# Kernel tuning notes

Hardware: AMD Instinct MI355X
Metric: run time of the kernel (lower is better)

The kernel has to match this reference:

```python
import jax, jax.numpy as jnp
import numpy as np

N_NODES = 50000
N_EDGES = 800000
D = 128
L = 3
BN_EPS = 1e-5


def _l2norm(x):
    # torch F.normalize(p=2, dim=-1): x / max(||x||, 1e-12)
    n = jnp.linalg.norm(x, axis=-1, keepdims=True)
    return x / jnp.maximum(n, 1e-12)


def setup_inputs() -> dict:
    key = jax.random.key(0)
    ks = jax.random.split(key, 5)
    x = jax.random.normal(ks[0], (N_NODES, D), dtype=jnp.float32)
    edge_index = jax.random.randint(ks[1], (2, N_EDGES), 0, N_NODES, dtype=jnp.int64)
    # stacked per-layer params; Linear stored as [in, out] (y = x @ W + b)
    W1 = jax.random.normal(ks[2], (L, D, D), dtype=jnp.float32) * 0.05
    W2 = jax.random.normal(ks[3], (L, D, D), dtype=jnp.float32) * 0.05
    b1 = jnp.zeros((L, D), jnp.float32)
    b2 = jnp.zeros((L, D), jnp.float32)
    gamma = jnp.ones((L, D), jnp.float32)
    beta = jnp.zeros((L, D), jnp.float32)
    eps = jnp.zeros((L,), jnp.float32)
    return {"x": x, "edge_index": edge_index, "W1": W1, "b1": b1,
            "gamma": gamma, "beta": beta, "W2": W2, "b2": b2, "eps": eps}


def _gin_layer(x, src, dst, W1, b1, g, be, W2, b2, eps):
    # message + scatter-add aggregation: sum_j x_j -> node i
    agg = jax.ops.segment_sum(x[src], dst, num_segments=N_NODES)
    # update(): L2 normalize aggregated messages
    agg = _l2norm(agg)
    # eps-weighted residual on L2-normalized root features
    out = agg + (1.0 + eps) * _l2norm(x)
    # MLP: Linear -> BatchNorm1d (training stats) -> ReLU -> Linear
    h = out @ W1 + b1
    mu = jnp.mean(h, axis=0)
    var = jnp.mean(jnp.square(h - mu), axis=0)  # biased var (torch BN training)
    h = g * (h - mu) * jax.lax.rsqrt(var + BN_EPS) + be
    h = jax.nn.relu(h)
    return h @ W2 + b2


def reference(x, edge_index, W1, b1, gamma, beta, W2, b2, eps):
    src, dst = edge_index[0], edge_index[1]
    for i in range(L):
        x = _gin_layer(x, src, dst, W1[i], b1[i], gamma[i], beta[i], W2[i], b2[i], eps[i])
        if i != L - 1:
            x = jax.nn.relu(x)
    return x
```

## Files before the change

kernel.cpp:

```cpp
#include <hip/hip_runtime.h>
#include <hip/hip_bf16.h>

#define N_NODES 50000
#define N_EDGES 800000
#define D 128
#define L_LAYERS 3
#define BN_EPS 1e-5f
#define NBUK 196
#define BIN_CHUNK 4096
#define NBIN_BLOCKS 196
#define BSTRIDE 5120
#define AROW 68

typedef __attribute__((ext_vector_type(8))) short short8;
typedef __attribute__((ext_vector_type(4))) float floatx4;
typedef __attribute__((ext_vector_type(4))) unsigned short ushort4v;

__device__ __forceinline__ unsigned short f2bf(float f) {
    unsigned u = __builtin_bit_cast(unsigned, f);
    u += 0x7FFFu + ((u >> 16) & 1u);
    return (unsigned short)(u >> 16);
}
__device__ __forceinline__ float bf2f(unsigned short h) {
    unsigned u = ((unsigned)h) << 16;
    return __builtin_bit_cast(float, u);
}
__device__ __forceinline__ float bf2f_lo(unsigned p) {
    return __builtin_bit_cast(float, p << 16);
}
__device__ __forceinline__ float bf2f_hi(unsigned p) {
    return __builtin_bit_cast(float, p & 0xFFFF0000u);
}

__device__ __forceinline__ int edge_at(const void* ei, const int* flag64, long long i) {
    if (*flag64) return (int)((const long long*)ei)[i];
    return ((const int*)ei)[i];
}

__global__ __launch_bounds__(256) void prep_kernel(const float* __restrict__ x,
        const void* __restrict__ ei, int* __restrict__ flag,
        const float* __restrict__ W1, const float* __restrict__ W2,
        short* __restrict__ Wp, unsigned short* __restrict__ xb,
        unsigned* __restrict__ zreg, int zwords) {
    int bid = blockIdx.x;
    int t = threadIdx.x;
    if (bid == 0) {
        __shared__ int nz;
        if (t == 0) nz = 0;
        __syncthreads();
        if (((const int*)ei)[2 * t + 1] != 0) atomicAdd(&nz, 1);
        __syncthreads();
        if (t == 0) *flag = (nz == 0) ? 1 : 0;
        for (int i = t; i < zwords; i += 256) zreg[i] = 0u;
    } else if (bid <= 48) {
        int tid = (bid - 1) * 256 + t;
        int mat = tid >> 11;
        int t2 = tid & 2047;
        int kt = t2 >> 9;
        int nt = (t2 >> 6) & 7;
        int lane = t2 & 63;
        const float* W = (mat < 3) ? (W1 + (size_t)mat * D * D)
                                   : (W2 + (size_t)(mat - 3) * D * D);
        int kbase = kt * 32 + (lane >> 4) * 8;
        int n = nt * 16 + (lane & 15);
        short8 frag;
        #pragma unroll
        for (int j = 0; j < 8; j++) frag[j] = (short)f2bf(W[(kbase + j) * D + n]);
        *(short8*)(Wp + (size_t)mat * D * D + (size_t)t2 * 8) = frag;
    } else {
        long long i = (long long)((bid - 49) * 256 + t) * 4;
        float4 v = *(const float4*)(x + i);
        ushort4v o;
        o.x = f2bf(v.x); o.y = f2bf(v.y); o.z = f2bf(v.z); o.w = f2bf(v.w);
        *(ushort4v*)(xb + i) = o;
    }
}

__global__ __launch_bounds__(256) void bin_kernel(const void* __restrict__ ei,
        const int* __restrict__ flag64, int* __restrict__ bucketCursor,
        unsigned* __restrict__ binned) {
    __shared__ int lhist[NBUK];
    __shared__ int gbase[NBUK];
    int t = threadIdx.x;
    for (int i = t; i < NBUK; i += 256) lhist[i] = 0;
    __syncthreads();

    int e0 = blockIdx.x * BIN_CHUNK;
    unsigned w[BIN_CHUNK / 256];
    short bkt[BIN_CHUNK / 256];
    short lidx[BIN_CHUNK / 256];
    #pragma unroll
    for (int i = 0; i < BIN_CHUNK / 256; i++) {
        int e = e0 + t + i * 256;
        if (e < N_EDGES) {
            int s = edge_at(ei, flag64, e);
            int d = edge_at(ei, flag64, (long long)N_EDGES + e);
            int b = d >> 8;
            w[i] = ((unsigned)s << 8) | (unsigned)(d & 255);
            bkt[i] = (short)b;
            lidx[i] = (short)atomicAdd(&lhist[b], 1);
        } else {
            bkt[i] = -1;
        }
    }
    __syncthreads();
    for (int i = t; i < NBUK; i += 256) {
        int c = lhist[i];
        gbase[i] = i * BSTRIDE + (c ? atomicAdd(&bucketCursor[i], c) : 0);
    }
    __syncthreads();
    #pragma unroll
    for (int i = 0; i < BIN_CHUNK / 256; i++) {
        if (bkt[i] >= 0)
            binned[gbase[bkt[i]] + (int)lidx[i]] = w[i];
    }
}

__global__ __launch_bounds__(256) void csr_build_kernel(const unsigned* __restrict__ binned,
        const int* __restrict__ bucketCursor, int* __restrict__ rowptr, int* __restrict__ csr) {
    __shared__ int ls[256];
    __shared__ int lhist[256];
    __shared__ int lcur[256];
    int b = blockIdx.x, t = threadIdx.x;
    int cv = (t < NBUK) ? bucketCursor[t] : 0;
    ls[t] = cv;
    __syncthreads();
    for (int off = 1; off < 256; off <<= 1) {
        int u = (t >= off) ? ls[t - off] : 0;
        __syncthreads();
        ls[t] += u;
        __syncthreads();
    }
    int base = (b == 0) ? 0 : ls[b - 1];
    int n = ls[b] - base;
    __syncthreads();

    lhist[t] = 0;
    __syncthreads();
    const unsigned* src = binned + (size_t)b * BSTRIDE;
    for (int i = t; i < n; i += 256)
        atomicAdd(&lhist[src[i] & 255u], 1);
    __syncthreads();
    int v = lhist[t];
    ls[t] = v;
    __syncthreads();
    for (int off = 1; off < 256; off <<= 1) {
        int u = (t >= off) ? ls[t - off] : 0;
        __syncthreads();
        ls[t] += u;
        __syncthreads();
    }
    int excl = ls[t] - v;
    int dst = b * 256 + t;
    if (dst <= N_NODES) rowptr[dst] = base + excl;
    lcur[t] = excl;
    __syncthreads();
    for (int i = t; i < n; i += 256) {
        unsigned wv = src[i];
        int pos = atomicAdd(&lcur[wv & 255u], 1);
        csr[base + pos] = (int)(wv >> 8);
    }
}

__global__ __launch_bounds__(1024) void gather_gemm1_kernel(
        const unsigned short* __restrict__ xb,
        const int* __restrict__ rowptr, const int* __restrict__ csr,
        const float* __restrict__ epsArr, int layer,
        const short* __restrict__ Wp, const float* __restrict__ b,
        unsigned* __restrict__ Hout,
        float* __restrict__ gsum, float* __restrict__ gsq) {
    __shared__ unsigned lA[64 * AROW];
    __shared__ float lsum2[2][D];
    __shared__ float lsq2[2][D];
    __shared__ int wq;

    int wave = threadIdx.x >> 6, lane = threadIdx.x & 63;
    int r0 = blockIdx.x * 64;
    float eps1 = 1.0f + epsArr[layer];
    if (threadIdx.x == 0) wq = 0;
    __syncthreads();

    for (;;) {
        int r;
        if (lane == 0) r = atomicAdd(&wq, 1);
        r = __shfl(r, 0);
        if (r >= 64) break;
        int row = r0 + r;
        unsigned pack = 0;
        if (row < N_NODES) {
            int beg = rowptr[row], end = rowptr[row + 1];
            float a0 = 0.f, a1 = 0.f, b0 = 0.f, b1 = 0.f;
            float c0 = 0.f, c1 = 0.f, d0 = 0.f, d1 = 0.f;
            for (int base = beg; base < end; base += 64) {
                int n = end - base;
                if (n > 64) n = 64;
                int idx = (lane < n) ? csr[base + lane] : 0;
                int j = 0;
                for (; j + 7 < n; j += 8) {
                    int s0 = __shfl(idx, j);
                    int s1 = __shfl(idx, j + 1);
                    int s2 = __shfl(idx, j + 2);
                    int s3 = __shfl(idx, j + 3);
                    int s4 = __shfl(idx, j + 4);
                    int s5 = __shfl(idx, j + 5);
                    int s6 = __shfl(idx, j + 6);
                    int s7 = __shfl(idx, j + 7);
                    unsigned p0 = *(const unsigned*)(xb + (long long)s0 * D + lane * 2);
                    unsigned p1 = *(const unsigned*)(xb + (long long)s1 * D + lane * 2);
                    unsigned p2 = *(const unsigned*)(xb + (long long)s2 * D + lane * 2);
                    unsigned p3 = *(const unsigned*)(xb + (long long)s3 * D + lane * 2);
                    unsigned p4 = *(const unsigned*)(xb + (long long)s4 * D + lane * 2);
                    unsigned p5 = *(const unsigned*)(xb + (long long)s5 * D + lane * 2);
                    unsigned p6 = *(const unsigned*)(xb + (long long)s6 * D + lane * 2);
                    unsigned p7 = *(const unsigned*)(xb + (long long)s7 * D + lane * 2);
                    a0 += bf2f_lo(p0); a1 += bf2f_hi(p0);
                    b0 += bf2f_lo(p1); b1 += bf2f_hi(p1);
                    c0 += bf2f_lo(p2); c1 += bf2f_hi(p2);
                    d0 += bf2f_lo(p3); d1 += bf2f_hi(p3);
                    a0 += bf2f_lo(p4); a1 += bf2f_hi(p4);
                    b0 += bf2f_lo(p5); b1 += bf2f_hi(p5);
                    c0 += bf2f_lo(p6); c1 += bf2f_hi(p6);
                    d0 += bf2f_lo(p7); d1 += bf2f_hi(p7);
                }
                for (; j + 3 < n; j += 4) {
                    int s0 = __shfl(idx, j);
                    int s1 = __shfl(idx, j + 1);
                    int s2 = __shfl(idx, j + 2);
                    int s3 = __shfl(idx, j + 3);
                    unsigned p0 = *(const unsigned*)(xb + (long long)s0 * D + lane * 2);
                    unsigned p1 = *(const unsigned*)(xb + (long long)s1 * D + lane * 2);
                    unsigned p2 = *(const unsigned*)(xb + (long long)s2 * D + lane * 2);
                    unsigned p3 = *(const unsigned*)(xb + (long long)s3 * D + lane * 2);
                    a0 += bf2f_lo(p0); a1 += bf2f_hi(p0);
                    b0 += bf2f_lo(p1); b1 += bf2f_hi(p1);
                    c0 += bf2f_lo(p2); c1 += bf2f_hi(p2);
                    d0 += bf2f_lo(p3); d1 += bf2f_hi(p3);
                }
                for (; j < n; j++) {
                    int s0 = __shfl(idx, j);
                    unsigned p0 = *(const unsigned*)(xb + (long long)s0 * D + lane * 2);
                    a0 += bf2f_lo(p0); a1 += bf2f_hi(p0);
                }
            }
            float ax = a0 + b0 + c0 + d0;
            float ay = a1 + b1 + c1 + d1;
            unsigned pself = *(const unsigned*)(xb + (long long)row * D + lane * 2);
            float xv0 = bf2f_lo(pself), xv1 = bf2f_hi(pself);
            float sa = ax * ax + ay * ay;
            float sx = xv0 * xv0 + xv1 * xv1;
            #pragma unroll
            for (int mm = 32; mm >= 1; mm >>= 1) {
                sa += __shfl_xor(sa, mm);
                sx += __shfl_xor(sx, mm);
            }
            float ra = 1.0f / fmaxf(sqrtf(sa), 1e-12f);
            float rx = eps1 / fmaxf(sqrtf(sx), 1e-12f);
            float ox = ax * ra + xv0 * rx;
            float oy = ay * ra + xv1 * rx;
            pack = (unsigned)f2bf(ox) | ((unsigned)f2bf(oy) << 16);
        }
        lA[r * AROW + lane] = pack;
    }
    __syncthreads();

    int m = lane & 15, g = lane >> 4;
    int nt = wave & 7, rg2 = wave >> 3;
    int col = nt * 16 + m;
    float bcol = b[col];

    short8 bfr[4];
    #pragma unroll
    for (int kt = 0; kt < 4; kt++)
        bfr[kt] = *(const short8*)(Wp + (size_t)((kt * 8 + nt) * 64 + lane) * 8);

    short8 a2[2][4];
    #pragma unroll
    for (int rt2 = 0; rt2 < 2; rt2++) {
        const unsigned* lbase = lA + ((rg2 * 2 + rt2) * 16 + m) * AROW;
        #pragma unroll
        for (int kt = 0; kt < 4; kt++)
            a2[rt2][kt] = *(const short8*)(lbase + kt * 16 + g * 4);
    }
    __syncthreads();

    unsigned short* hlds = (unsigned short*)lA;
    float s = 0.f, q = 0.f;
    #pragma unroll
    for (int rt2 = 0; rt2 < 2; rt2++) {
        int rt = rg2 * 2 + rt2;
        floatx4 acc = (floatx4){0.f, 0.f, 0.f, 0.f};
        #pragma unroll
        for (int kt = 0; kt < 4; kt++)
            acc = __builtin_amdgcn_mfma_f32_16x16x32_bf16(a2[rt2][kt], bfr[kt], acc, 0, 0, 0);
        #pragma unroll
        for (int r = 0; r < 4; r++) {
            int lrow = rt * 16 + g * 4 + r;
            int grow = r0 + lrow;
            float h = acc[r] + bcol;
            hlds[lrow * (AROW * 2) + col] = f2bf(h);
            if (grow < N_NODES) { s += h; q += h * h; }
        }
    }
    s += __shfl_xor(s, 16); s += __shfl_xor(s, 32);
    q += __shfl_xor(q, 16); q += __shfl_xor(q, 32);
    if (lane < 16) { lsum2[rg2][col] = s; lsq2[rg2][col] = q; }
    __syncthreads();

    {
        int crow = threadIdx.x >> 4;
        int cq = threadIdx.x & 15;
        if (r0 + crow < N_NODES) {
            uint4 v = *(const uint4*)(lA + crow * AROW + cq * 4);
            *(uint4*)(Hout + (size_t)(r0 + crow) * 64 + cq * 4) = v;
        }
    }
    if (threadIdx.x < D) {
        atomicAdd(&gsum[threadIdx.x], lsum2[0][threadIdx.x] + lsum2[1][threadIdx.x]);
        atomicAdd(&gsq[threadIdx.x], lsq2[0][threadIdx.x] + lsq2[1][threadIdx.x]);
    }
}

__global__ __launch_bounds__(256) void gemm2_mfma_kernel(const unsigned short* __restrict__ H,
        const float* __restrict__ gsum, const float* __restrict__ gsq,
        const float* __restrict__ gamma, const float* __restrict__ beta,
        const short* __restrict__ Wp, const float* __restrict__ b,
        float* __restrict__ Yf32, unsigned* __restrict__ Yb16, int finalLayer) {
    __shared__ float s_scale[D];
    __shared__ float s_shift[D];
    __shared__ unsigned so[64 * 132];
    if (threadIdx.x < D) {
        int c = threadIdx.x;
        const float invN = 1.0f / (float)N_NODES;
        float mu = gsum[c] * invN;
        float var = fmaxf(gsq[c] * invN - mu * mu, 0.f);
        float is = rsqrtf(var + BN_EPS);
        float sc = gamma[c] * is;
        s_scale[c] = sc;
        s_shift[c] = beta[c] - mu * sc;
    }
    __syncthreads();

    int wave = threadIdx.x >> 6, lane = threadIdx.x & 63;
    int r0 = blockIdx.x * 64;
    int m = lane & 15, g = lane >> 4;
    int arow = r0 + wave * 16 + m;
    bool valid = arow < N_NODES;

    short8 a[4];
    #pragma unroll
    for (int kt = 0; kt < 4; kt++) {
        int koff = kt * 32 + g * 8;
        if (valid) {
            short8 hv = *(const short8*)(H + (long long)arow * D + koff);
            #pragma unroll
            for (int j = 0; j < 8; j++) {
                float h = bf2f((unsigned short)hv[j]);
                float v = fmaxf(h * s_scale[koff + j] + s_shift[koff + j], 0.f);
                a[kt][j] = (short)f2bf(v);
            }
        } else {
            a[kt] = (short8)0;
        }
    }

    floatx4 acc[8];
    #pragma unroll
    for (int nt = 0; nt < 8; nt++) acc[nt] = (floatx4){0.f, 0.f, 0.f, 0.f};

    #pragma unroll
    for (int nt = 0; nt < 8; nt++) {
        #pragma unroll
        for (int kt = 0; kt < 4; kt++) {
            short8 bf = *(const short8*)(Wp + (size_t)((kt * 8 + nt) * 64 + lane) * 8);
            acc[nt] = __builtin_amdgcn_mfma_f32_16x16x32_bf16(a[kt], bf, acc[nt], 0, 0, 0);
        }
    }

    if (finalLayer) {
        unsigned short dummy;
        (void)dummy;
        float* sof = (float*)so;
        #pragma unroll
        for (int nt = 0; nt < 8; nt++) {
            int col = nt * 16 + m;
            float bcol = b[col];
            #pragma unroll
            for (int r = 0; r < 4; r++) {
                int lrow = wave * 16 + g * 4 + r;
                sof[lrow * 132 + col] = acc[nt][r] + bcol;
            }
        }
        __syncthreads();
        #pragma unroll
        for (int k = 0; k < 8; k++) {
            int c = threadIdx.x + k * 256;
            int crow = c >> 5;
            int cq = c & 31;
            if (r0 + crow < N_NODES) {
                float4 v = *(const float4*)(sof + crow * 132 + cq * 4);
                *(float4*)(Yf32 + (size_t)(r0 + crow) * D + cq * 4) = v;
            }
        }
    } else {
        unsigned short* sos = (unsigned short*)so;
        #pragma unroll
        for (int nt = 0; nt < 8; nt++) {
            int col = nt * 16 + m;
            float bcol = b[col];
            #pragma unroll
            for (int r = 0; r < 4; r++) {
                int lrow = wave * 16 + g * 4 + r;
                sos[lrow * (AROW * 2) + col] = f2bf(fmaxf(acc[nt][r] + bcol, 0.f));
            }
        }
        __syncthreads();
        #pragma unroll
        for (int k = 0; k < 4; k++) {
            int c = threadIdx.x + k * 256;
            int crow = c >> 4;
            int cq = c & 15;
            if (r0 + crow < N_NODES) {
                uint4 v = *(const uint4*)(so + crow * AROW + cq * 4);
                *(uint4*)(Yb16 + (size_t)(r0 + crow) * 64 + cq * 4) = v;
            }
        }
    }
}

extern "C" void kernel_launch(void* const* d_in, const int* in_sizes, int n_in,
                              void* d_out, int out_size, void* d_ws, size_t ws_size,
                              hipStream_t stream) {
    const float* x      = (const float*)d_in[0];
    const void*  ei     = d_in[1];
    const float* W1     = (const float*)d_in[2];
    const float* b1     = (const float*)d_in[3];
    const float* gamma  = (const float*)d_in[4];
    const float* beta   = (const float*)d_in[5];
    const float* W2     = (const float*)d_in[6];
    const float* b2     = (const float*)d_in[7];
    const float* epsArr = (const float*)d_in[8];
    float* out = (float*)d_out;

    char* ws = (char*)d_ws;
    const size_t hbuf = (size_t)N_NODES * D * sizeof(short);
    unsigned short* Xb  = (unsigned short*)ws;
    unsigned* H16       = (unsigned*)(ws + hbuf);
    char* p             = ws + 2 * hbuf;
    short* Wp       = (short*)p;         p += 6 * (size_t)D * D * sizeof(short);
    int* rowptr     = (int*)p;           p += (N_NODES + 1) * sizeof(int);
    int* csr        = (int*)p;           p += N_EDGES * sizeof(int);
    unsigned* binned= (unsigned*)p;      p += (size_t)NBUK * BSTRIDE * sizeof(unsigned);
    int* flag       = (int*)p;           p += sizeof(int);
    char* zbase     = p;
    int* bucketCursor=(int*)p;           p += NBUK * sizeof(int);
    float* stats    = (float*)p;         p += (size_t)L_LAYERS * 2 * D * sizeof(float);
    int zwords      = (int)((p - zbase) / 4);

    prep_kernel<<<1 + 48 + (N_NODES * D / 4) / 256, 256, 0, stream>>>(
        x, ei, flag, W1, W2, Wp, Xb, (unsigned*)zbase, zwords);

    bin_kernel<<<NBIN_BLOCKS, 256, 0, stream>>>(ei, flag, bucketCursor, binned);
    csr_build_kernel<<<NBUK, 256, 0, stream>>>(binned, bucketCursor, rowptr, csr);

    const int gemmGrid = (N_NODES + 63) / 64;
    for (int l = 0; l < L_LAYERS; l++) {
        int fin = (l == L_LAYERS - 1) ? 1 : 0;
        float* gsum = stats + (size_t)l * 2 * D;
        float* gsq  = gsum + D;

        gather_gemm1_kernel<<<gemmGrid, 1024, 0, stream>>>(
            Xb, rowptr, csr, epsArr, l,
            Wp + (size_t)l * D * D, b1 + (size_t)l * D,
            H16, gsum, gsq);
        gemm2_mfma_kernel<<<gemmGrid, 256, 0, stream>>>(
            (const unsigned short*)H16, gsum, gsq,
            gamma + (size_t)l * D, beta + (size_t)l * D,
            Wp + (size_t)(3 + l) * D * D, b2 + (size_t)l * D,
            out, (unsigned*)Xb, fin);
    }
}
```

Before: 246.0 us.

## Gather four neighbors per wave with 16-byte loads and padded CSR buckets

The gather now splits each wave into four 16-lane groups. Each group loads a whole 256-byte bf16 row with uint4 loads, so one step fetches four neighbors, and the CSR stores byte offsets directly. CSR buckets use a fixed stride and each row is padded to a multiple of four edges with a pointer to a zero row appended to Xb. The fused gather+GEMM1 kernel moves from 1024-thread/64-row blocks to 256-thread/16-row blocks, and BN statistics are spread over 8 partitioned atomic slots to cut contention. In exchange there is more padding work and more, smaller blocks, and gemm2 must reduce the partial statistics.

```diff
diff --git a/kernel.cpp b/kernel.cpp
--- a/kernel.cpp
+++ b/kernel.cpp
@@ -10,7 +10,10 @@
 #define BIN_CHUNK 4096
 #define NBIN_BLOCKS 196
 #define BSTRIDE 5120
+#define CSTRIDE 5376
 #define AROW 68
+#define NPART 8
+#define PADOFF (N_NODES << 8)
 
 typedef __attribute__((ext_vector_type(8))) short short8;
 typedef __attribute__((ext_vector_type(4))) float floatx4;
@@ -52,6 +55,7 @@
         __syncthreads();
         if (t == 0) *flag = (nz == 0) ? 1 : 0;
         for (int i = t; i < zwords; i += 256) zreg[i] = 0u;
+        if (t < 64) ((unsigned*)(xb + (size_t)N_NODES * D))[t] = 0u;
     } else if (bid <= 48) {
         int tid = (bid - 1) * 256 + t;
         int mat = tid >> 11;
@@ -117,13 +121,23 @@
 }
 
 __global__ __launch_bounds__(256) void csr_build_kernel(const unsigned* __restrict__ binned,
-        const int* __restrict__ bucketCursor, int* __restrict__ rowptr, int* __restrict__ csr) {
+        const int* __restrict__ bucketCursor, int* __restrict__ rowptr,
+        int* __restrict__ bucketEnd, int* __restrict__ csr) {
     __shared__ int ls[256];
     __shared__ int lhist[256];
     __shared__ int lcur[256];
     int b = blockIdx.x, t = threadIdx.x;
-    int cv = (t < NBUK) ? bucketCursor[t] : 0;
-    ls[t] = cv;
+    int n = bucketCursor[b];
+    const unsigned* src = binned + (size_t)b * BSTRIDE;
+
+    lhist[t] = 0;
+    __syncthreads();
+    for (int i = t; i < n; i += 256)
+        atomicAdd(&lhist[src[i] & 255u], 1);
+    __syncthreads();
+    int c = lhist[t];
+    int pc = (c + 3) & ~3;
+    ls[t] = pc;
     __syncthreads();
     for (int off = 1; off < 256; off <<= 1) {
         int u = (t >= off) ? ls[t - off] : 0;
@@ -131,51 +145,38 @@
         ls[t] += u;
         __syncthreads();
     }
-    int base = (b == 0) ? 0 : ls[b - 1];
-    int n = ls[b] - base;
-    __syncthreads();
-
-    lhist[t] = 0;
-    __syncthreads();
-    const unsigned* src = binned + (size_t)b * BSTRIDE;
-    for (int i = t; i < n; i += 256)
-        atomicAdd(&lhist[src[i] & 255u], 1);
-    __syncthreads();
-    int v = lhist[t];
-    ls[t] = v;
-    __syncthreads();
-    for (int off = 1; off < 256; off <<= 1) {
-        int u = (t >= off) ? ls[t - off] : 0;
-        __syncthreads();
-        ls[t] += u;
-        __syncthreads();
-    }
-    int excl = ls[t] - v;
+    int excl = ls[t] - pc;
+    int base = b * CSTRIDE;
     int dst = b * 256 + t;
     if (dst <= N_NODES) rowptr[dst] = base + excl;
+    if (t == 0) bucketEnd[b] = base + ls[255];
     lcur[t] = excl;
     __syncthreads();
     for (int i = t; i < n; i += 256) {
         unsigned wv = src[i];
         int pos = atomicAdd(&lcur[wv & 255u], 1);
-        csr[base + pos] = (int)(wv >> 8);
-    }
-}
-
-__global__ __launch_bounds__(1024) void gather_gemm1_kernel(
+        csr[base + pos] = (int)(wv & 0xFFFFFF00u);
+    }
+    __syncthreads();
+    for (int i = lcur[t]; i < excl + pc; i++)
+        csr[base + i] = PADOFF;
+}
+
+__global__ __launch_bounds__(256, 8) void gather_gemm1_kernel(
         const unsigned short* __restrict__ xb,
         const int* __restrict__ rowptr, const int* __restrict__ csr,
+        const int* __restrict__ bucketEnd,
         const float* __restrict__ epsArr, int layer,
-        const short* __restrict__ Wp, const float* __restrict__ b,
+        const short* __restrict__ Wp, const float* __restrict__ bB,
         unsigned* __restrict__ Hout,
         float* __restrict__ gsum, float* __restrict__ gsq) {
-    __shared__ unsigned lA[64 * AROW];
-    __shared__ float lsum2[2][D];
-    __shared__ float lsq2[2][D];
+    __shared__ __attribute__((aligned(16))) unsigned lA[16 * AROW];
     __shared__ int wq;
-
+    const char* xbase = (const char*)xb;
     int wave = threadIdx.x >> 6, lane = threadIdx.x & 63;
-    int r0 = blockIdx.x * 64;
+    int g = lane >> 4, p = lane & 15;
+    unsigned po = (unsigned)(p << 4);
+    int r0 = blockIdx.x * 16;
     float eps1 = 1.0f + epsArr[layer];
     if (threadIdx.x == 0) wq = 0;
     __syncthreads();
@@ -184,139 +185,124 @@
         int r;
         if (lane == 0) r = atomicAdd(&wq, 1);
         r = __shfl(r, 0);
-        if (r >= 64) break;
+        if (r >= 16) break;
         int row = r0 + r;
-        unsigned pack = 0;
-        if (row < N_NODES) {
-            int beg = rowptr[row], end = rowptr[row + 1];
-            float a0 = 0.f, a1 = 0.f, b0 = 0.f, b1 = 0.f;
-            float c0 = 0.f, c1 = 0.f, d0 = 0.f, d1 = 0.f;
-            for (int base = beg; base < end; base += 64) {
-                int n = end - base;
-                if (n > 64) n = 64;
-                int idx = (lane < n) ? csr[base + lane] : 0;
-                int j = 0;
-                for (; j + 7 < n; j += 8) {
-                    int s0 = __shfl(idx, j);
-                    int s1 = __shfl(idx, j + 1);
-                    int s2 = __shfl(idx, j + 2);
-                    int s3 = __shfl(idx, j + 3);
-                    int s4 = __shfl(idx, j + 4);
-                    int s5 = __shfl(idx, j + 5);
-                    int s6 = __shfl(idx, j + 6);
-                    int s7 = __shfl(idx, j + 7);
-                    unsigned p0 = *(const unsigned*)(xb + (long long)s0 * D + lane * 2);
-                    unsigned p1 = *(const unsigned*)(xb + (long long)s1 * D + lane * 2);
-                    unsigned p2 = *(const unsigned*)(xb + (long long)s2 * D + lane * 2);
-                    unsigned p3 = *(const unsigned*)(xb + (long long)s3 * D + lane * 2);
-                    unsigned p4 = *(const unsigned*)(xb + (long long)s4 * D + lane * 2);
-                    unsigned p5 = *(const unsigned*)(xb + (long long)s5 * D + lane * 2);
-                    unsigned p6 = *(const unsigned*)(xb + (long long)s6 * D + lane * 2);
-                    unsigned p7 = *(const unsigned*)(xb + (long long)s7 * D + lane * 2);
-                    a0 += bf2f_lo(p0); a1 += bf2f_hi(p0);
-                    b0 += bf2f_lo(p1); b1 += bf2f_hi(p1);
-                    c0 += bf2f_lo(p2); c1 += bf2f_hi(p2);
-                    d0 += bf2f_lo(p3); d1 += bf2f_hi(p3);
-                    a0 += bf2f_lo(p4); a1 += bf2f_hi(p4);
-                    b0 += bf2f_lo(p5); b1 += bf2f_hi(p5);
-                    c0 += bf2f_lo(p6); c1 += bf2f_hi(p6);
-                    d0 += bf2f_lo(p7); d1 += bf2f_hi(p7);
-                }
-                for (; j + 3 < n; j += 4) {
-                    int s0 = __shfl(idx, j);
-                    int s1 = __shfl(idx, j + 1);
-                    int s2 = __shfl(idx, j + 2);
-                    int s3 = __shfl(idx, j + 3);
-                    unsigned p0 = *(const unsigned*)(xb + (long long)s0 * D + lane * 2);
-                    unsigned p1 = *(const unsigned*)(xb + (long long)s1 * D + lane * 2);
-                    unsigned p2 = *(const unsigned*)(xb + (long long)s2 * D + lane * 2);
-                    unsigned p3 = *(const unsigned*)(xb + (long long)s3 * D + lane * 2);
-                    a0 += bf2f_lo(p0); a1 += bf2f_hi(p0);
-                    b0 += bf2f_lo(p1); b1 += bf2f_hi(p1);
-                    c0 += bf2f_lo(p2); c1 += bf2f_hi(p2);
-                    d0 += bf2f_lo(p3); d1 += bf2f_hi(p3);
-                }
-                for (; j < n; j++) {
-                    int s0 = __shfl(idx, j);
-                    unsigned p0 = *(const unsigned*)(xb + (long long)s0 * D + lane * 2);
-                    a0 += bf2f_lo(p0); a1 += bf2f_hi(p0);
-                }
-            }
-            float ax = a0 + b0 + c0 + d0;
-            float ay = a1 + b1 + c1 + d1;
-            unsigned pself = *(const unsigned*)(xb + (long long)row * D + lane * 2);
-            float xv0 = bf2f_lo(pself), xv1 = bf2f_hi(pself);
-            float sa = ax * ax + ay * ay;
-            float sx = xv0 * xv0 + xv1 * xv1;
-            #pragma unroll
-            for (int mm = 32; mm >= 1; mm >>= 1) {
-                sa += __shfl_xor(sa, mm);
-                sx += __shfl_xor(sx, mm);
-            }
-            float ra = 1.0f / fmaxf(sqrtf(sa), 1e-12f);
-            float rx = eps1 / fmaxf(sqrtf(sx), 1e-12f);
-            float ox = ax * ra + xv0 * rx;
-            float oy = ay * ra + xv1 * rx;
-            pack = (unsigned)f2bf(ox) | ((unsigned)f2bf(oy) << 16);
-        }
-        lA[r * AROW + lane] = pack;
-    }
-    __syncthreads();
-
-    int m = lane & 15, g = lane >> 4;
-    int nt = wave & 7, rg2 = wave >> 3;
-    int col = nt * 16 + m;
-    float bcol = b[col];
-
-    short8 bfr[4];
+        int beg = rowptr[row];
+        int end = ((row & 255) == 255) ? bucketEnd[row >> 8] : rowptr[row + 1];
+        float ac[8];
+        #pragma unroll
+        for (int k = 0; k < 8; k++) ac[k] = 0.f;
+        for (int base = beg; base < end; base += 64) {
+            int n = end - base;
+            if (n > 64) n = 64;
+            unsigned idxv = (lane < n) ? (unsigned)csr[base + lane] : (unsigned)PADOFF;
+            int j = 0;
+            for (; j + 8 <= n; j += 8) {
+                unsigned o0 = (unsigned)__shfl((int)idxv, j + g) + po;
+                unsigned o1 = (unsigned)__shfl((int)idxv, j + 4 + g) + po;
+                uint4 v0 = *(const uint4*)(xbase + o0);
+                uint4 v1 = *(const uint4*)(xbase + o1);
+                ac[0] += bf2f_lo(v0.x); ac[1] += bf2f_hi(v0.x);
+                ac[2] += bf2f_lo(v0.y); ac[3] += bf2f_hi(v0.y);
+                ac[4] += bf2f_lo(v0.z); ac[5] += bf2f_hi(v0.z);
+                ac[6] += bf2f_lo(v0.w); ac[7] += bf2f_hi(v0.w);
+                ac[0] += bf2f_lo(v1.x); ac[1] += bf2f_hi(v1.x);
+                ac[2] += bf2f_lo(v1.y); ac[3] += bf2f_hi(v1.y);
+                ac[4] += bf2f_lo(v1.z); ac[5] += bf2f_hi(v1.z);
+                ac[6] += bf2f_lo(v1.w); ac[7] += bf2f_hi(v1.w);
+            }
+            if (j < n) {
+                unsigned o0 = (unsigned)__shfl((int)idxv, j + g) + po;
+                uint4 v0 = *(const uint4*)(xbase + o0);
+                ac[0] += bf2f_lo(v0.x); ac[1] += bf2f_hi(v0.x);
+                ac[2] += bf2f_lo(v0.y); ac[3] += bf2f_hi(v0.y);
+                ac[4] += bf2f_lo(v0.z); ac[5] += bf2f_hi(v0.z);
+                ac[6] += bf2f_lo(v0.w); ac[7] += bf2f_hi(v0.w);
+            }
+        }
+        #pragma unroll
+        for (int k = 0; k < 8; k++) {
+            ac[k] += __shfl_xor(ac[k], 16);
+            ac[k] += __shfl_xor(ac[k], 32);
+        }
+        uint4 sv = *(const uint4*)(xbase + (((unsigned)row << 8) + po));
+        float xv[8];
+        xv[0] = bf2f_lo(sv.x); xv[1] = bf2f_hi(sv.x);
+        xv[2] = bf2f_lo(sv.y); xv[3] = bf2f_hi(sv.y);
+        xv[4] = bf2f_lo(sv.z); xv[5] = bf2f_hi(sv.z);
+        xv[6] = bf2f_lo(sv.w); xv[7] = bf2f_hi(sv.w);
+        float sa = 0.f, sx = 0.f;
+        #pragma unroll
+        for (int k = 0; k < 8; k++) { sa += ac[k] * ac[k]; sx += xv[k] * xv[k]; }
+        #pragma unroll
+        for (int mm = 8; mm >= 1; mm >>= 1) {
+            sa += __shfl_xor(sa, mm);
+            sx += __shfl_xor(sx, mm);
+        }
+        float ra = 1.0f / fmaxf(sqrtf(sa), 1e-12f);
+        float rx = eps1 / fmaxf(sqrtf(sx), 1e-12f);
+        unsigned wds[4];
+        #pragma unroll
+        for (int k = 0; k < 4; k++) {
+            float lo = ac[2 * k] * ra + xv[2 * k] * rx;
+            float hi = ac[2 * k + 1] * ra + xv[2 * k + 1] * rx;
+            wds[k] = (unsigned)f2bf(lo) | ((unsigned)f2bf(hi) << 16);
+        }
+        if (g == 0)
+            *(uint4*)(lA + r * AROW + p * 4) = make_uint4(wds[0], wds[1], wds[2], wds[3]);
+    }
+    __syncthreads();
+
+    int m = p;
+    int nt0 = wave * 2, nt1 = nt0 + 1;
+    short8 afr[4];
     #pragma unroll
     for (int kt = 0; kt < 4; kt++)
-        bfr[kt] = *(const short8*)(Wp + (size_t)((kt * 8 + nt) * 64 + lane) * 8);
-
-    short8 a2[2][4];
-    #pragma unroll
-    for (int rt2 = 0; rt2 < 2; rt2++) {
-        const unsigned* lbase = lA + ((rg2 * 2 + rt2) * 16 + m) * AROW;
-        #pragma unroll
-        for (int kt = 0; kt < 4; kt++)
-            a2[rt2][kt] = *(const short8*)(lbase + kt * 16 + g * 4);
-    }
-    __syncthreads();
+        afr[kt] = *(const short8*)(lA + m * AROW + kt * 16 + g * 4);
+    __syncthreads();
+
+    floatx4 acc0 = (floatx4){0.f, 0.f, 0.f, 0.f};
+    floatx4 acc1 = (floatx4){0.f, 0.f, 0.f, 0.f};
+    #pragma unroll
+    for (int kt = 0; kt < 4; kt++) {
+        short8 bf0 = *(const short8*)(Wp + (size_t)((kt * 8 + nt0) * 64 + lane) * 8);
+        short8 bf1 = *(const short8*)(Wp + (size_t)((kt * 8 + nt1) * 64 + lane) * 8);
+        acc0 = __builtin_amdgcn_mfma_f32_16x16x32_bf16(afr[kt], bf0, acc0, 0, 0, 0);
+        acc1 = __builtin_amdgcn_mfma_f32_16x16x32_bf16(afr[kt], bf1, acc1, 0, 0, 0);
+    }
 
     unsigned short* hlds = (unsigned short*)lA;
-    float s = 0.f, q = 0.f;
-    #pragma unroll
-    for (int rt2 = 0; rt2 < 2; rt2++) {
-        int rt = rg2 * 2 + rt2;
-        floatx4 acc = (floatx4){0.f, 0.f, 0.f, 0.f};
-        #pragma unroll
-        for (int kt = 0; kt < 4; kt++)
-            acc = __builtin_amdgcn_mfma_f32_16x16x32_bf16(a2[rt2][kt], bfr[kt], acc, 0, 0, 0);
-        #pragma unroll
-        for (int r = 0; r < 4; r++) {
-            int lrow = rt * 16 + g * 4 + r;
-            int grow = r0 + lrow;
-            float h = acc[r] + bcol;
-            hlds[lrow * (AROW * 2) + col] = f2bf(h);
-            if (grow < N_NODES) { s += h; q += h * h; }
-        }
-    }
-    s += __shfl_xor(s, 16); s += __shfl_xor(s, 32);
-    q += __shfl_xor(q, 16); q += __shfl_xor(q, 32);
-    if (lane < 16) { lsum2[rg2][col] = s; lsq2[rg2][col] = q; }
+    float bc0 = bB[nt0 * 16 + m], bc1 = bB[nt1 * 16 + m];
+    float s0 = 0.f, q0 = 0.f, s1 = 0.f, q1 = 0.f;
+    #pragma unroll
+    for (int r = 0; r < 4; r++) {
+        int lrow = g * 4 + r;
+        float h0 = acc0[r] + bc0;
+        float h1 = acc1[r] + bc1;
+        hlds[lrow * (AROW * 2) + nt0 * 16 + m] = f2bf(h0);
+        hlds[lrow * (AROW * 2) + nt1 * 16 + m] = f2bf(h1);
+        s0 += h0; q0 += h0 * h0;
+        s1 += h1; q1 += h1 * h1;
+    }
+    s0 += __shfl_xor(s0, 16); s0 += __shfl_xor(s0, 32);
+    q0 += __shfl_xor(q0, 16); q0 += __shfl_xor(q0, 32);
+    s1 += __shfl_xor(s1, 16); s1 += __shfl_xor(s1, 32);
+    q1 += __shfl_xor(q1, 16); q1 += __shfl_xor(q1, 32);
+    if (lane < 16) {
+        float* gs = gsum + (size_t)(blockIdx.x & (NPART - 1)) * D;
+        float* gq = gsq + (size_t)(blockIdx.x & (NPART - 1)) * D;
+        atomicAdd(&gs[nt0 * 16 + m], s0);
+        atomicAdd(&gs[nt1 * 16 + m], s1);
+        atomicAdd(&gq[nt0 * 16 + m], q0);
+        atomicAdd(&gq[nt1 * 16 + m], q1);
+    }
     __syncthreads();
 
     {
         int crow = threadIdx.x >> 4;
         int cq = threadIdx.x & 15;
-        if (r0 + crow < N_NODES) {
-            uint4 v = *(const uint4*)(lA + crow * AROW + cq * 4);
-            *(uint4*)(Hout + (size_t)(r0 + crow) * 64 + cq * 4) = v;
-        }
-    }
-    if (threadIdx.x < D) {
-        atomicAdd(&gsum[threadIdx.x], lsum2[0][threadIdx.x] + lsum2[1][threadIdx.x]);
-        atomicAdd(&gsq[threadIdx.x], lsq2[0][threadIdx.x] + lsq2[1][threadIdx.x]);
+        uint4 v = *(const uint4*)(lA + crow * AROW + cq * 4);
+        *(uint4*)(Hout + (size_t)(r0 + crow) * 64 + cq * 4) = v;
     }
 }
 
@@ -331,8 +317,14 @@
     if (threadIdx.x < D) {
         int c = threadIdx.x;
         const float invN = 1.0f / (float)N_NODES;
-        float mu = gsum[c] * invN;
-        float var = fmaxf(gsq[c] * invN - mu * mu, 0.f);
+        float su = 0.f, sq = 0.f;
+        #pragma unroll
+        for (int pp = 0; pp < NPART; pp++) {
+            su += gsum[(size_t)pp * D + c];
+            sq += gsq[(size_t)pp * D + c];
+        }
+        float mu = su * invN;
+        float var = fmaxf(sq * invN - mu * mu, 0.f);
         float is = rsqrtf(var + BN_EPS);
         float sc = gamma[c] * is;
         s_scale[c] = sc;
@@ -377,8 +369,6 @@
     }
 
     if (finalLayer) {
-        unsigned short dummy;
-        (void)dummy;
         float* sof = (float*)so;
         #pragma unroll
         for (int nt = 0; nt < 8; nt++) {
@@ -442,37 +432,40 @@
     float* out = (float*)d_out;
 
     char* ws = (char*)d_ws;
+    const size_t xbuf = (size_t)(N_NODES + 1) * D * sizeof(short);
     const size_t hbuf = (size_t)N_NODES * D * sizeof(short);
     unsigned short* Xb  = (unsigned short*)ws;
-    unsigned* H16       = (unsigned*)(ws + hbuf);
-    char* p             = ws + 2 * hbuf;
+    unsigned* H16       = (unsigned*)(ws + xbuf);
+    char* p             = ws + xbuf + hbuf;
     short* Wp       = (short*)p;         p += 6 * (size_t)D * D * sizeof(short);
     int* rowptr     = (int*)p;           p += (N_NODES + 1) * sizeof(int);
-    int* csr        = (int*)p;           p += N_EDGES * sizeof(int);
+    int* csr        = (int*)p;           p += (size_t)NBUK * CSTRIDE * sizeof(int);
     unsigned* binned= (unsigned*)p;      p += (size_t)NBUK * BSTRIDE * sizeof(unsigned);
+    int* bucketEnd  = (int*)p;           p += NBUK * sizeof(int);
     int* flag       = (int*)p;           p += sizeof(int);
     char* zbase     = p;
     int* bucketCursor=(int*)p;           p += NBUK * sizeof(int);
-    float* stats    = (float*)p;         p += (size_t)L_LAYERS * 2 * D * sizeof(float);
+    float* stats    = (float*)p;         p += (size_t)L_LAYERS * 2 * NPART * D * sizeof(float);
     int zwords      = (int)((p - zbase) / 4);
 
     prep_kernel<<<1 + 48 + (N_NODES * D / 4) / 256, 256, 0, stream>>>(
         x, ei, flag, W1, W2, Wp, Xb, (unsigned*)zbase, zwords);
 
     bin_kernel<<<NBIN_BLOCKS, 256, 0, stream>>>(ei, flag, bucketCursor, binned);
-    csr_build_kernel<<<NBUK, 256, 0, stream>>>(binned, bucketCursor, rowptr, csr);
-
-    const int gemmGrid = (N_NODES + 63) / 64;
+    csr_build_kernel<<<NBUK, 256, 0, stream>>>(binned, bucketCursor, rowptr, bucketEnd, csr);
+
+    const int g1Grid = N_NODES / 16;
+    const int g2Grid = (N_NODES + 63) / 64;
     for (int l = 0; l < L_LAYERS; l++) {
         int fin = (l == L_LAYERS - 1) ? 1 : 0;
-        float* gsum = stats + (size_t)l * 2 * D;
-        float* gsq  = gsum + D;
-
-        gather_gemm1_kernel<<<gemmGrid, 1024, 0, stream>>>(
-            Xb, rowptr, csr, epsArr, l,
+        float* gsum = stats + (size_t)l * 2 * NPART * D;
+        float* gsq  = gsum + (size_t)NPART * D;
+
+        gather_gemm1_kernel<<<g1Grid, 256, 0, stream>>>(
+            Xb, rowptr, csr, bucketEnd, epsArr, l,
             Wp + (size_t)l * D * D, b1 + (size_t)l * D,
             H16, gsum, gsq);
-        gemm2_mfma_kernel<<<gemmGrid, 256, 0, stream>>>(
+        gemm2_mfma_kernel<<<g2Grid, 256, 0, stream>>>(
             (const unsigned short*)H16, gsum, gsq,
             gamma + (size_t)l * D, beta + (size_t)l * D,
             Wp + (size_t)(3 + l) * D * D, b2 + (size_t)l * D,
```

New measurement: 210.3 us. 14.5% less time.
